# Optimization experiments

Hardware: AMD Instinct MI355X
Metric: run time of the kernel (lower is better)

The kernel has to match this reference:

```python
import jax, jax.numpy as jnp
import numpy as np
from jax import lax

B, T, IDIM, HDIM = 128, 256, 64, 128
TS, KS, OC1, ANF = 64, 3, 100, 64
S1 = TS - 3 * (KS - 1)   # 58: three VALID ks=3 stride-1 convs
S = S1 * S1              # 3364
HN = 2 * HDIM            # 256 = h_dim * l_dim (l_dim=2)
F = S + HN               # 3620
HID = F // 2             # 1810


def _conv(x, w, b):
    y = lax.conv_general_dilated(x, w, (1, 1), 'VALID',
                                 dimension_numbers=('NCHW', 'OIHW', 'NCHW'))
    return y + b[None, :, None, None]


def _lstm_layer(x, w_ih, w_hh, b_ih, b_hh):
    # x: [B, T, D] -> (outputs [B, T, H], final hidden [B, H]); PyTorch gate order i,f,g,o
    Bn = x.shape[0]
    h0 = jnp.zeros((Bn, HDIM), x.dtype)
    c0 = jnp.zeros((Bn, HDIM), x.dtype)
    def step(carry, xt):
        h, c = carry
        g = xt @ w_ih.T + h @ w_hh.T + b_ih + b_hh
        i, f, gg, o = jnp.split(g, 4, axis=-1)
        c = jax.nn.sigmoid(f) * c + jax.nn.sigmoid(i) * jnp.tanh(gg)
        h = jax.nn.sigmoid(o) * jnp.tanh(c)
        return (h, c), h
    (hT, cT), ys = lax.scan(step, (h0, c0), jnp.swapaxes(x, 0, 1))
    return jnp.swapaxes(ys, 0, 1), hT


def setup_inputs() -> dict:
    key = jax.random.key(0)
    k = jax.random.split(key, 30)
    s = 0.05
    H4 = 4 * HDIM
    return {
        'x1': jax.random.normal(k[0], (B, 3, TS, TS), jnp.float32),
        'x2': jax.random.normal(k[1], (B, T, IDIM), jnp.float32),
        # conv2a/conv2b: two Monte-Carlo weight samples of the same Bayesian conv2 layer
        'conv1_w': jax.random.normal(k[2], (OC1, 3, KS, KS), jnp.float32) * s,
        'conv1_b': jax.random.normal(k[3], (OC1,), jnp.float32) * s,
        'conv2a_w': jax.random.normal(k[4], (OC1, OC1, KS, KS), jnp.float32) * s,
        'conv2a_b': jax.random.normal(k[5], (OC1,), jnp.float32) * s,
        'conv2b_w': jax.random.normal(k[6], (OC1, OC1, KS, KS), jnp.float32) * s,
        'conv2b_b': jax.random.normal(k[7], (OC1,), jnp.float32) * s,
        'w_ih0': jax.random.normal(k[8], (H4, IDIM), jnp.float32) * s,
        'w_hh0': jax.random.normal(k[9], (H4, HDIM), jnp.float32) * s,
        'b_ih0': jax.random.normal(k[10], (H4,), jnp.float32) * s,
        'b_hh0': jax.random.normal(k[11], (H4,), jnp.float32) * s,
        'w_ih1': jax.random.normal(k[12], (H4, HDIM), jnp.float32) * s,
        'w_hh1': jax.random.normal(k[13], (H4, HDIM), jnp.float32) * s,
        'b_ih1': jax.random.normal(k[14], (H4,), jnp.float32) * s,
        'b_hh1': jax.random.normal(k[15], (H4,), jnp.float32) * s,
        'attn1_w': jax.random.normal(k[16], (ANF, F), jnp.float32) * s,
        'attn1_b': jax.random.normal(k[17], (ANF,), jnp.float32) * s,
        'attn2_w': jax.random.normal(k[18], (1, ANF), jnp.float32) * s,
        'attn2_b': jax.random.normal(k[19], (1,), jnp.float32) * s,
        'fc1_w': jax.random.normal(k[20], (HID, F), jnp.float32) * s,
        'fc1_b': jax.random.normal(k[21], (HID,), jnp.float32) * s,
        'fc2_w': jax.random.normal(k[22], (1, HID), jnp.float32) * s,
        'fc2_b': jax.random.normal(k[23], (1,), jnp.float32) * s,
    }


def reference(x1, x2, conv1_w, conv1_b, conv2a_w, conv2a_b, conv2b_w, conv2b_b,
              w_ih0, w_hh0, b_ih0, b_hh0, w_ih1, w_hh1, b_ih1, b_hh1,
              attn1_w, attn1_b, attn2_w, attn2_b, fc1_w, fc1_b, fc2_w, fc2_b):
    Bn = x1.shape[0]
    # CNN branch
    x = jax.nn.relu(_conv(x1, conv1_w, conv1_b))
    x = jax.nn.relu(_conv(x, conv2a_w, conv2a_b))
    x = jax.nn.relu(_conv(x, conv2b_w, conv2b_b))
    xd = x.reshape(Bn, OC1, S)                               # [B, oc1, S]
    # LSTM branch (2 layers, dropout in eval mode = identity)
    y0, h0f = _lstm_layer(x2, w_ih0, w_hh0, b_ih0, b_hh0)
    _, h1f = _lstm_layer(y0, w_ih1, w_hh1, b_ih1, b_hh1)
    hn = jnp.concatenate([h0f, h1f], axis=1)                 # [B, 2*h_dim]
    # Broadcast hidden state across channels (replaces the torch concat loop)
    hn_b = jnp.broadcast_to(hn[:, None, :], (Bn, OC1, HN))
    fused = jnp.concatenate([xd, hn_b], axis=2)              # [B, oc1, F]
    # Attention
    a = jnp.tanh(fused @ attn1_w.T + attn1_b)                # [B, oc1, anf]
    a = a @ attn2_w.T + attn2_b                              # [B, oc1, 1]
    a = jax.nn.softmax(a, axis=1)
    ctx = jnp.einsum('bcs,bco->bso', xd, a).reshape(Bn, S)   # [B, S]
    # Fusion MLP (dropout eval-mode identity)
    m = jnp.concatenate([ctx, hn], axis=1)                   # [B, F]
    h = jax.nn.relu(m @ fc1_w.T + fc1_b)
    return h @ fc2_w.T + fc2_b                               # [B, 1]
```

## Files before the change

### kernel.cpp

```cpp
#include <hip/hip_runtime.h>
#include <hip/hip_bf16.h>
#include <math.h>

#define BB 128
#define TT 256
#define IDIM 64
#define HD 128
#define G4 512
#define OC 100
#define W1 62
#define W2 60
#define W3 58
#define NPX1 (W1*W1)
#define NPX2 (W2*W2)
#define NPX3 (W3*W3)
#define SS NPX3
#define FF (SS + 2*HD)
#define HIDN 1810
#define ANF 64

typedef __hip_bfloat16 bf16;
typedef _Float16 f16;
typedef __attribute__((ext_vector_type(8))) short bf16x8;
typedef __attribute__((ext_vector_type(4))) short bf16x4;
typedef __attribute__((ext_vector_type(2))) _Float16 half2v;
typedef __attribute__((ext_vector_type(4))) float f32x4;

__device__ __forceinline__ float ldf(const float* p) { return *p; }
__device__ __forceinline__ float ldf(const bf16* p)  { return __bfloat162float(*p); }
__device__ __forceinline__ void  stf(float* p, float v) { *p = v; }
__device__ __forceinline__ void  stf(bf16* p, float v)  { *p = __float2bfloat16(v); }

__device__ __forceinline__ short f2bs(float v) {
    bf16 t = __float2bfloat16(v); short s; __builtin_memcpy(&s, &t, 2); return s;
}
__device__ __forceinline__ float fsig(float x) {
    return __builtin_amdgcn_rcpf(1.f + __expf(-x));
}
__device__ __forceinline__ float ftanh(float x) {
    float t = __expf(-2.f * fabsf(x));
    float r = __builtin_amdgcn_rcpf(1.f + t);
    float m = 1.f - 2.f * t * r;
    return copysignf(m, x);
}
__device__ __forceinline__ float fmix2(unsigned w, unsigned h, float acc) {
    half2v wv, hv;
    __builtin_memcpy(&wv, &w, 4);
    __builtin_memcpy(&hv, &h, 4);
    acc = fmaf((float)wv[0], (float)hv[0], acc);
    acc = fmaf((float)wv[1], (float)hv[1], acc);
    return acc;
}

__device__ __forceinline__ bf16x8 load8(const bf16* p) { return *(const bf16x8*)p; }
__device__ __forceinline__ bf16x8 load8(const float* p) {
    float4 x = *(const float4*)p;
    float4 y = *(const float4*)(p + 4);
    bf16x8 r;
    r[0] = f2bs(x.x); r[1] = f2bs(x.y); r[2] = f2bs(x.z); r[3] = f2bs(x.w);
    r[4] = f2bs(y.x); r[5] = f2bs(y.y); r[6] = f2bs(y.z); r[7] = f2bs(y.w);
    return r;
}

__global__ void zero_kernel(float* o, int n)
{
    int i = blockIdx.x * 256 + threadIdx.x;
    if (i < n) o[i] = 0.f;
}

__global__ __launch_bounds__(256)
void cvt4_bf16(const float* __restrict__ s, bf16* __restrict__ d, int n4)
{
    int i = blockIdx.x * 256 + threadIdx.x;
    if (i >= n4) return;
    float4 v = ((const float4*)s)[i];
    bf16x4 o;
    o[0] = f2bs(v.x); o[1] = f2bs(v.y); o[2] = f2bs(v.z); o[3] = f2bs(v.w);
    *(bf16x4*)(d + 4 * (size_t)i) = o;
}

__global__ __launch_bounds__(256)
void cvt4_f16(const float* __restrict__ s, f16* __restrict__ d, int n4)
{
    int i = blockIdx.x * 256 + threadIdx.x;
    if (i >= n4) return;
    float4 v = ((const float4*)s)[i];
    f16 o[4] = {(f16)v.x, (f16)v.y, (f16)v.z, (f16)v.w};
    *(uint2*)(d + 4 * (size_t)i) = *(uint2*)o;
}

__global__ __launch_bounds__(256)
void conv1_kernel(const float* __restrict__ x1,
                  const float* __restrict__ w,
                  const float* __restrict__ bias,
                  bf16* __restrict__ out)
{
    __shared__ float wl[2700];
    __shared__ float bl[OC];
    int tid = threadIdx.x;
    for (int i = tid; i < 2700; i += 256) wl[i] = w[i];
    if (tid < OC) bl[tid] = bias[tid];
    __syncthreads();
    int b  = blockIdx.x;
    int px = blockIdx.y * 256 + tid;
    if (px >= NPX1) return;
    int y = px / W1, x = px % W1;
    float in[3][3][3];
    const float* xb = x1 + (size_t)b * 3 * 64 * 64;
#pragma unroll
    for (int ic = 0; ic < 3; ic++)
#pragma unroll
        for (int r = 0; r < 3; r++)
#pragma unroll
            for (int c = 0; c < 3; c++)
                in[ic][r][c] = xb[(ic * 64 + y + r) * 64 + x + c];
    bf16* ob = out + (size_t)b * OC * NPX1 + px;
    for (int oc = 0; oc < OC; ++oc) {
        float acc = bl[oc];
        const float* wp = &wl[oc * 27];
#pragma unroll
        for (int ic = 0; ic < 3; ic++)
#pragma unroll
            for (int r = 0; r < 3; r++)
#pragma unroll
                for (int c = 0; c < 3; c++)
                    acc = fmaf(in[ic][r][c], wp[ic * 9 + r * 3 + c], acc);
        ob[(size_t)oc * NPX1] = __float2bfloat16(fmaxf(acc, 0.f));
    }
}

__global__ __launch_bounds__(256)
void wt_repack(const float* __restrict__ w, bf16* __restrict__ WT)
{
    int idx = blockIdx.x * 256 + threadIdx.x;
    if (idx >= 129024) return;
    int i  = idx & 31;
    int oc = (idx >> 5) % 112;
    int ts = idx / (112 * 32);
    int s = ts & 3, t = ts >> 2;
    int ic = s * 32 + i;
    float v = 0.f;
    if (oc < OC && ic < OC) v = w[(oc * OC + ic) * 9 + t];
    WT[idx] = __float2bfloat16(v);
}

__global__ __launch_bounds__(512, 1)
void conv2_mfma(const bf16* __restrict__ in,
                const bf16* __restrict__ WT,
                const float* __restrict__ bias,
                bf16* __restrict__ out,
                int iw, int ow)
{
    __shared__ bf16 il[10 * 72 * 40];
    __shared__ bf16 wl[4032 * 8];
    int tid = threadIdx.x;
    int b = blockIdx.x;
    int y0 = blockIdx.y * 8;
    int wid = tid >> 6;
    int l = tid & 63;
    int hq = l >> 4;
    int l16 = l & 15;
    int yo = y0 + wid;

    f32x4 acc[7][4];
#pragma unroll
    for (int f = 0; f < 7; f++) {
#pragma unroll
        for (int r = 0; r < 4; r++) {
            int oc = f * 16 + hq * 4 + r;
            float bv = (oc < OC) ? bias[oc] : 0.f;
#pragma unroll
            for (int n = 0; n < 4; n++) acc[f][n][r] = bv;
        }
    }

    const size_t ims = (size_t)iw * iw;
    int icl = tid & 31;
    int t2  = tid >> 5;
    for (int s = 0; s < 4; ++s) {
        __syncthreads();
        int ic = s * 32 + icl;
        bool icok = ic < OC;
        const bf16* ibase = in + (size_t)(b * OC + ic) * ims;
#pragma unroll
        for (int it = 0; it < 6; ++it) {
            int u2 = t2 + it * 16;
            if (u2 < 90) {
                int r = u2 / 9, xb = u2 - r * 9;
                int x8 = xb * 8;
                int yy = y0 + r;
                bf16x8 v = {0, 0, 0, 0, 0, 0, 0, 0};
                if (icok && yy < iw && x8 < iw) {
                    const short* sp = (const short*)(ibase + (size_t)yy * iw + x8);
                    if (x8 + 8 <= iw) {
                        const unsigned* sp32 = (const unsigned*)sp;
#pragma unroll
                        for (int q = 0; q < 4; q++)
                            ((unsigned*)&v)[q] = sp32[q];
                    } else {
                        for (int k = 0; k < 8; k++)
                            if (x8 + k < iw) ((short*)&v)[k] = sp[k];
                    }
                }
                bf16* dst = &il[(r * 72 + x8) * 40 + icl];
#pragma unroll
                for (int k = 0; k < 8; k++)
                    *(short*)&dst[k * 40] = ((short*)&v)[k];
            }
        }
#pragma unroll
        for (int it = 0; it < 8; ++it) {
            int u = tid + it * 512;
            if (u < 4032) {
                int t = u / 448; int rem = u - t * 448;
                int oc = rem >> 2; int hq2 = rem & 3;
                *(bf16x8*)&wl[(size_t)((t * 4 + hq2) * 112 + oc) * 8] =
                    *(const bf16x8*)(WT + (size_t)((t * 4 + s) * 112 + oc) * 32 + hq2 * 8);
            }
        }
        __syncthreads();

#pragma unroll
        for (int ky = 0; ky < 3; ++ky) {
#pragma unroll
            for (int kx = 0; kx < 3; ++kx) {
                int t = ky * 3 + kx;
                bf16x8 a[7];
#pragma unroll
                for (int f = 0; f < 7; f++)
                    a[f] = *(const bf16x8*)&wl[(size_t)((t * 4 + hq) * 112 + f * 16 + l16) * 8];
                bf16x8 bfr[4];
#pragma unroll
                for (int n = 0; n < 4; n++)
                    bfr[n] = *(const bf16x8*)&il[((wid + ky) * 72 + kx + l16 + n * 16) * 40 + hq * 8];
#pragma unroll
                for (int f = 0; f < 7; f++)
#pragma unroll
                    for (int n = 0; n < 4; n++)
                        acc[f][n] = __builtin_amdgcn_mfma_f32_16x16x32_bf16(
                            a[f], bfr[n], acc[f][n], 0, 0, 0);
            }
        }
    }

    if (yo < ow) {
#pragma unroll
        for (int f = 0; f < 7; f++) {
#pragma unroll
            for (int r = 0; r < 4; r++) {
                int oc = f * 16 + hq * 4 + r;
                if (oc < OC) {
#pragma unroll
                    for (int n = 0; n < 4; n++) {
                        int x = n * 16 + l16;
                        if (x < ow)
                            out[((size_t)(b * OC + oc) * ow + yo) * ow + x] =
                                __float2bfloat16(fmaxf(acc[f][n][r], 0.f));
                    }
                }
            }
        }
    }
}

template<typename TB, typename TC, int ACT>
__global__ __launch_bounds__(256)
void gemm_mfma(const bf16* __restrict__ A, int lda,
               const TB* __restrict__ B, int ldb,
               const float* __restrict__ bias,
               TC* __restrict__ C, int ldc,
               int M, int N, int K)
{
    __shared__ bf16 As[64 * 72];
    __shared__ bf16 Bs[64 * 72];
    int tid = threadIdx.x;
    int l = tid & 63, wid = tid >> 6;
    int l16 = l & 15, h = l >> 4;
    int m0 = blockIdx.x * 64, n0 = blockIdx.y * 64;
    f32x4 acc[4];
#pragma unroll
    for (int nb = 0; nb < 4; nb++) acc[nb] = (f32x4){0.f, 0.f, 0.f, 0.f};

    int rs = tid >> 3;
    int kc = (tid & 7) * 8;

    for (int k0 = 0; k0 < K; k0 += 64) {
        int kr = K - k0;
#pragma unroll
        for (int half = 0; half < 2; half++) {
            int rr = rs + half * 32;
            bf16x8 av = {0, 0, 0, 0, 0, 0, 0, 0};
            int m = m0 + rr;
            if (m < M) {
                const short* src = (const short*)(A + (size_t)m * lda + k0 + kc);
                if (kc + 8 <= kr) av = *(const bf16x8*)src;
                else if (kc < kr) {
                    for (int j = 0; j < 8; j++) if (kc + j < kr) ((short*)&av)[j] = src[j];
                }
            }
            *(bf16x8*)&As[rr * 72 + kc] = av;
            bf16x8 bv = {0, 0, 0, 0, 0, 0, 0, 0};
            int n = n0 + rr;
            if (n < N) {
                const TB* src = B + (size_t)n * ldb + k0 + kc;
                if (kc + 8 <= kr) bv = load8(src);
                else if (kc < kr) {
                    for (int j = 0; j < 8; j++) if (kc + j < kr) ((short*)&bv)[j] = f2bs(ldf(src + j));
                }
            }
            *(bf16x8*)&Bs[rr * 72 + kc] = bv;
        }
        __syncthreads();
#pragma unroll
        for (int kk = 0; kk < 2; kk++) {
            bf16x8 af = *(const bf16x8*)&As[(wid * 16 + l16) * 72 + kk * 32 + h * 8];
#pragma unroll
            for (int nb = 0; nb < 4; nb++) {
                bf16x8 bfr = *(const bf16x8*)&Bs[(nb * 16 + l16) * 72 + kk * 32 + h * 8];
                acc[nb] = __builtin_amdgcn_mfma_f32_16x16x32_bf16(af, bfr, acc[nb], 0, 0, 0);
            }
        }
        __syncthreads();
    }
#pragma unroll
    for (int nb = 0; nb < 4; nb++) {
        int col = n0 + nb * 16 + l16;
        if (col >= N) continue;
        float bv = bias ? bias[col] : 0.f;
#pragma unroll
        for (int reg = 0; reg < 4; reg++) {
            int row = m0 + wid * 16 + h * 4 + reg;
            if (row < M) {
                float v = acc[nb][reg] + bv;
                if (ACT == 1) v = fmaxf(v, 0.f);
                stf(&C[(size_t)row * ldc + col], v);
            }
        }
    }
}

template<typename TA, typename TC, int BM, int BN, int BK, int TM, int TN, int ACT>
__global__ __launch_bounds__((BM / TM) * (BN / TN))
void gemm_tn(const TA* __restrict__ A, int lda,
             const float* __restrict__ Bmat, int ldb,
             const float* __restrict__ bias,
             TC* __restrict__ C, int ldc,
             int M, int N, int K)
{
    constexpr int TX = BN / TN;
    constexpr int TY = BM / TM;
    constexpr int NT = TX * TY;
    __shared__ float As[BK][BM + 1];
    __shared__ float Bs[BK][BN + 1];
    int tid = threadIdx.x;
    int tx = tid % TX, ty = tid / TX;
    int m0 = blockIdx.x * BM, n0 = blockIdx.y * BN;
    float acc[TM][TN] = {};
    for (int k0 = 0; k0 < K; k0 += BK) {
        for (int idx = tid; idx < BM * BK; idx += NT) {
            int i = idx / BK, j = idx % BK;
            int m = m0 + i, k = k0 + j;
            As[j][i] = (m < M && k < K) ? ldf(&A[(size_t)m * lda + k]) : 0.f;
        }
        for (int idx = tid; idx < BN * BK; idx += NT) {
            int i = idx / BK, j = idx % BK;
            int n = n0 + i, k = k0 + j;
            Bs[j][i] = (n < N && k < K) ? Bmat[(size_t)n * ldb + k] : 0.f;
        }
        __syncthreads();
#pragma unroll
        for (int k = 0; k < BK; ++k) {
            float av[TM], bv[TN];
#pragma unroll
            for (int i = 0; i < TM; i++) av[i] = As[k][ty * TM + i];
#pragma unroll
            for (int j = 0; j < TN; j++) bv[j] = Bs[k][tx * TN + j];
#pragma unroll
            for (int i = 0; i < TM; i++)
#pragma unroll
                for (int j = 0; j < TN; j++)
                    acc[i][j] += av[i] * bv[j];
        }
        __syncthreads();
    }
#pragma unroll
    for (int i = 0; i < TM; i++) {
        int m = m0 + ty * TM + i;
        if (m >= M) continue;
#pragma unroll
        for (int j = 0; j < TN; j++) {
            int n = n0 + tx * TN + j;
            if (n >= N) continue;
            float v = acc[i][j] + (bias ? bias[n] : 0.f);
            if (ACT == 1) v = fmaxf(v, 0.f);
            stf(&C[(size_t)m * ldc + n], v);
        }
    }
}

__global__ __launch_bounds__(512, 1)
void lstm_recur(const bf16* __restrict__ G,
                const f16* __restrict__ LWr,
                bf16* __restrict__ Y,
                float* __restrict__ HN,
                int hoff)
{
    __shared__ __align__(16) f16 hl[HD];
    __shared__ float ex[G4];
    int g = threadIdx.x;
    int b = blockIdx.x;
    uint4 wv[16];
    const uint4* wp = (const uint4*)(LWr + (size_t)g * HD);
#pragma unroll
    for (int q = 0; q < 16; q++) wv[q] = wp[q];
#pragma unroll
    for (int q = 0; q < 16; q++)
        asm volatile("" : "+v"(wv[q].x), "+v"(wv[q].y), "+v"(wv[q].z), "+v"(wv[q].w));
    float c = 0.f;
    if (g < HD) hl[g] = (f16)0.f;
    __syncthreads();
    const bf16* Gb = G + (size_t)b * TT * G4 + g;
    for (int t = 0; t < TT; ++t) {
        float dot = __bfloat162float(Gb[(size_t)t * G4]);
        float a0 = 0.f, a1 = 0.f, a2 = 0.f, a3 = 0.f;
#pragma unroll
        for (int q = 0; q < 16; q++) {
            uint4 hw = *(const uint4*)&hl[q * 8];
            a0 = fmix2(wv[q].x, hw.x, a0);
            a1 = fmix2(wv[q].y, hw.y, a1);
            a2 = fmix2(wv[q].z, hw.z, a2);
            a3 = fmix2(wv[q].w, hw.w, a3);
        }
        dot += (a0 + a1) + (a2 + a3);
        float tr;
        if (g < 2 * HD || g >= 3 * HD) tr = fsig(dot);
        else tr = ftanh(dot);
        ex[g] = tr;
        __syncthreads();
        if (g < HD) {
            float iv = ex[g], fv = ex[HD + g], gv = ex[2 * HD + g], ov = ex[3 * HD + g];
            c = fv * c + iv * gv;
            float nh = ov * ftanh(c);
            hl[g] = (f16)nh;
            if (Y) Y[((size_t)b * TT + t) * HD + g] = __float2bfloat16(nh);
            if (t == TT - 1) HN[(size_t)b * 256 + hoff + g] = nh;
        }
        __syncthreads();
    }
}

__global__ void bias_sum(const float* a, const float* b, float* o, int n)
{
    int i = blockIdx.x * 256 + threadIdx.x;
    if (i < n) o[i] = a[i] + b[i];
}

__global__ __launch_bounds__(128)
void attn_softmax(const float* __restrict__ T1,
                  const float* __restrict__ HB,
                  const float* __restrict__ a2w,
                  const float* __restrict__ a2b,
                  float* __restrict__ ATT)
{
    __shared__ float hbl[ANF];
    __shared__ float awl[ANF];
    __shared__ float red[128];
    int b = blockIdx.x, tid = threadIdx.x;
    if (tid < ANF) { hbl[tid] = HB[b * ANF + tid]; awl[tid] = a2w[tid]; }
    __syncthreads();
    float lg = -1e30f;
    if (tid < OC) {
        const float* tp = T1 + (size_t)(b * OC + tid) * ANF;
        float s = 0.f;
#pragma unroll 4
        for (int j = 0; j < ANF; j++) s += ftanh(tp[j] + hbl[j]) * awl[j];
        lg = s + a2b[0];
    }
    red[tid] = lg; __syncthreads();
    for (int st = 64; st > 0; st >>= 1) { if (tid < st) red[tid] = fmaxf(red[tid], red[tid + st]); __syncthreads(); }
    float mx = red[0]; __syncthreads();
    float e = (tid < OC) ? __expf(lg - mx) : 0.f;
    red[tid] = e; __syncthreads();
    for (int st = 64; st > 0; st >>= 1) { if (tid < st) red[tid] += red[tid + st]; __syncthreads(); }
    if (tid < OC) ATT[b * OC + tid] = e / red[0];
}

__global__ __launch_bounds__(256)
void ctx_concat(const bf16* __restrict__ XD,
                const float* __restrict__ ATT,
                const float* __restrict__ HN,
                bf16* __restrict__ M)
{
    __shared__ float al[OC];
    int b = blockIdx.x;
    int tid = threadIdx.x;
    if (tid < OC) al[tid] = ATT[b * OC + tid];
    __syncthreads();
    int s = blockIdx.y * 256 + tid;
    if (s < SS) {
        const bf16* xp = XD + (size_t)b * OC * SS + s;
        float acc = 0.f;
#pragma unroll 4
        for (int c = 0; c < OC; c++) acc = fmaf(__bfloat162float(xp[(size_t)c * SS]), al[c], acc);
        M[(size_t)b * FF + s] = __float2bfloat16(acc);
    } else if (s < FF) {
        M[(size_t)b * FF + s] = __float2bfloat16(HN[b * 256 + (s - SS)]);
    }
}

__global__ __launch_bounds__(256)
void fc2_kernel(const float* __restrict__ H1,
                const float* __restrict__ w,
                const float* __restrict__ bias,
                float* __restrict__ out)
{
    int tid = threadIdx.x;
    int lane = tid & 63, wid = tid >> 6;
    int b = blockIdx.x * 4 + wid;
    float acc = 0.f;
    for (int j = lane; j < HIDN; j += 64) acc = fmaf(H1[(size_t)b * HIDN + j], w[j], acc);
#pragma unroll
    for (int off = 32; off > 0; off >>= 1) acc += __shfl_down(acc, off, 64);
    if (lane == 0) out[b] = acc + bias[0];
}

extern "C" void kernel_launch(void* const* d_in, const int* in_sizes, int n_in,
                              void* d_out, int out_size, void* d_ws, size_t ws_size,
                              hipStream_t stream)
{
    const float* x1   = (const float*)d_in[0];
    const float* x2   = (const float*)d_in[1];
    const float* c1w  = (const float*)d_in[2];
    const float* c1b  = (const float*)d_in[3];
    const float* c2aw = (const float*)d_in[4];
    const float* c2ab = (const float*)d_in[5];
    const float* c2bw = (const float*)d_in[6];
    const float* c2bb = (const float*)d_in[7];
    const float* wih0 = (const float*)d_in[8];
    const float* whh0 = (const float*)d_in[9];
    const float* bih0 = (const float*)d_in[10];
    const float* bhh0 = (const float*)d_in[11];
    const float* wih1 = (const float*)d_in[12];
    const float* whh1 = (const float*)d_in[13];
    const float* bih1 = (const float*)d_in[14];
    const float* bhh1 = (const float*)d_in[15];
    const float* a1w  = (const float*)d_in[16];
    const float* a1b  = (const float*)d_in[17];
    const float* a2w  = (const float*)d_in[18];
    const float* a2b  = (const float*)d_in[19];
    const float* f1w  = (const float*)d_in[20];
    const float* f1b  = (const float*)d_in[21];
    const float* f2w  = (const float*)d_in[22];
    const float* f2b  = (const float*)d_in[23];
    float* out = (float*)d_out;

    char* base = (char*)d_ws;
    bf16* G0    = (bf16*)(base + 0);
    bf16* Y0    = (bf16*)(base + 33554432);
    bf16* G1    = G0;
    bf16* X2B   = (bf16*)(base + 41943040);
    bf16* WIH0B = (bf16*)(base + 46137344);
    bf16* WIH1B = (bf16*)(base + 46202880);
    f16*  LWf0  = (f16*)(base + 46333952);
    f16*  LWf1  = (f16*)(base + 46465024);
    const size_t LSTM_END = 46596096;

    int nb = 0; size_t ov = 0;
    for (int cand = BB; cand >= 32; cand >>= 1) {
        size_t cnn = (size_t)cand * OC * (NPX1 + NPX2) * 2;
        size_t o = cnn > LSTM_END ? cnn : LSTM_END;
        size_t q = o + 2048 + 2048 + 131072 + 32768
                 + (size_t)cand * OC * 64 * 4
                 + (((size_t)cand * OC * 4 + 255) & ~(size_t)255)
                 + 926720 + 926720 + 258048 + 258048 + 463360;
        if (ws_size >= q) { nb = cand; ov = o; break; }
    }
    if (nb == 0) {
        zero_kernel<<<1, 128, 0, stream>>>(out, out_size);
        return;
    }
    bf16* A1c = (bf16*)(base + 0);
    bf16* A2c = (bf16*)(base + (size_t)nb * OC * NPX1 * 2);
    bf16* XDc = A1c;
    size_t p = ov;
    float* BS0  = (float*)(base + p); p += 2048;
    float* BS1  = (float*)(base + p); p += 2048;
    float* HN   = (float*)(base + p); p += 131072;
    float* HB   = (float*)(base + p); p += 32768;
    float* T1c  = (float*)(base + p); p += (size_t)nb * OC * 64 * 4;
    float* ATTc = (float*)(base + p); p += ((size_t)nb * OC * 4 + 255) & ~(size_t)255;
    bf16*  MBb  = (bf16*)(base + p); p += 926720;
    float* H1   = (float*)(base + p); p += 926720;
    bf16* WTa   = (bf16*)(base + p); p += 258048;
    bf16* WTb   = (bf16*)(base + p); p += 258048;
    bf16* A1WB  = (bf16*)(base + p); p += 463360;

    wt_repack<<<504, 256, 0, stream>>>(c2aw, WTa);
    wt_repack<<<504, 256, 0, stream>>>(c2bw, WTb);
    cvt4_f16<<<64,   256, 0, stream>>>(whh0, LWf0, 16384);
    cvt4_f16<<<64,   256, 0, stream>>>(whh1, LWf1, 16384);
    cvt4_bf16<<<2048, 256, 0, stream>>>(x2,   X2B,   524288);
    cvt4_bf16<<<32,   256, 0, stream>>>(wih0, WIH0B, 8192);
    cvt4_bf16<<<64,   256, 0, stream>>>(wih1, WIH1B, 16384);
    cvt4_bf16<<<227,  256, 0, stream>>>(a1w,  A1WB,  57920);
    bias_sum<<<2, 256, 0, stream>>>(bih0, bhh0, BS0, G4);
    bias_sum<<<2, 256, 0, stream>>>(bih1, bhh1, BS1, G4);

    gemm_mfma<bf16, bf16, 0><<<dim3(512, 8), 256, 0, stream>>>(
        X2B, IDIM, WIH0B, IDIM, BS0, G0, G4, BB * TT, G4, IDIM);
    lstm_recur<<<BB, 512, 0, stream>>>(G0, LWf0, Y0, HN, 0);
    gemm_mfma<bf16, bf16, 0><<<dim3(512, 8), 256, 0, stream>>>(
        Y0, HD, WIH1B, HD, BS1, G1, G4, BB * TT, G4, HD);
    lstm_recur<<<BB, 512, 0, stream>>>(G1, LWf1, (bf16*)nullptr, HN, HD);

    gemm_tn<float, float, 32, 32, 16, 2, 2, 0><<<dim3(4, 2), 256, 0, stream>>>(
        HN, 256, a1w + SS, FF, a1b, HB, ANF, BB, ANF, 256);

    for (int c0 = 0; c0 < BB; c0 += nb) {
        conv1_kernel<<<dim3(nb, 16), 256, 0, stream>>>(
            x1 + (size_t)c0 * 3 * 64 * 64, c1w, c1b, A1c);
        conv2_mfma<<<dim3(nb, 8), 512, 0, stream>>>(A1c, WTa, c2ab, A2c, W1, W2);
        conv2_mfma<<<dim3(nb, 8), 512, 0, stream>>>(A2c, WTb, c2bb, XDc, W2, W3);
        gemm_mfma<bf16, float, 0><<<dim3(nb * OC / 64, 1), 256, 0, stream>>>(
            XDc, SS, A1WB, FF, nullptr, T1c, ANF, nb * OC, ANF, SS);
        attn_softmax<<<nb, 128, 0, stream>>>(T1c, HB + (size_t)c0 * ANF, a2w, a2b, ATTc);
        ctx_concat<<<dim3(nb, 15), 256, 0, stream>>>(
            XDc, ATTc, HN + (size_t)c0 * 256, MBb + (size_t)c0 * FF);
    }

    gemm_mfma<float, float, 1><<<dim3(2, 29), 256, 0, stream>>>(
        MBb, FF, f1w, FF, f1b, H1, HIDN, BB, HIDN, FF);
    fc2_kernel<<<BB / 4, 256, 0, stream>>>(H1, f2w, f2b, out);
}
```

Measured before the change: 1.229 ms.

## Double-buffer LSTM state to drop a barrier; relayout conv weight LDS tiles

The LSTM recurrence now keeps double-buffered hidden-state and gate arrays in shared memory, so each timestep needs only one __syncthreads instead of two. Every wave redundantly computes the cell update for two hidden units per lane, and only wave 0 writes the outputs. Separately, the conv kernel stores its weight tile in LDS in MFMA fragment order, so each lane reads contiguous 16-byte chunks, which is meant to cut bank conflicts. The cost is redundant cell-state arithmetic in all eight waves and extra shared memory.

Result: no change. 1.241 ms (+0.9%).

```diff
diff --git a/kernel.cpp b/kernel.cpp
--- a/kernel.cpp
+++ b/kernel.cpp
@@ -212,9 +212,11 @@
         for (int it = 0; it < 8; ++it) {
             int u = tid + it * 512;
             if (u < 4032) {
-                int t = u / 448; int rem = u - t * 448;
-                int oc = rem >> 2; int hq2 = rem & 3;
-                *(bf16x8*)&wl[(size_t)((t * 4 + hq2) * 112 + oc) * 8] =
+                int tf = u >> 6; int lp = u & 63;
+                int t = tf / 7, f = tf - t * 7;
+                int oc = f * 16 + (lp & 15);
+                int hq2 = lp >> 4;
+                *(bf16x8*)&wl[(size_t)u * 8] =
                     *(const bf16x8*)(WT + (size_t)((t * 4 + s) * 112 + oc) * 32 + hq2 * 8);
             }
         }
@@ -228,7 +230,7 @@
                 bf16x8 a[7];
 #pragma unroll
                 for (int f = 0; f < 7; f++)
-                    a[f] = *(const bf16x8*)&wl[(size_t)((t * 4 + hq) * 112 + f * 16 + l16) * 8];
+                    a[f] = *(const bf16x8*)&wl[(size_t)((t * 7 + f) * 64 + l) * 8];
                 bf16x8 bfr[4];
 #pragma unroll
                 for (int n = 0; n < 4; n++)
@@ -405,10 +407,12 @@
                 float* __restrict__ HN,
                 int hoff)
 {
-    __shared__ __align__(16) f16 hl[HD];
-    __shared__ float ex[G4];
+    __shared__ __align__(16) f16 hbuf[2][HD];
+    __shared__ __align__(16) float ex[2][G4];
     int g = threadIdx.x;
     int b = blockIdx.x;
+    int lane = g & 63;
+    int w = g >> 6;
     uint4 wv[16];
     const uint4* wp = (const uint4*)(LWr + (size_t)g * HD);
 #pragma unroll
@@ -416,16 +420,19 @@
 #pragma unroll
     for (int q = 0; q < 16; q++)
         asm volatile("" : "+v"(wv[q].x), "+v"(wv[q].y), "+v"(wv[q].z), "+v"(wv[q].w));
-    float c = 0.f;
-    if (g < HD) hl[g] = (f16)0.f;
+    float c0 = 0.f, c1 = 0.f;
+    if (g < HD) hbuf[0][g] = (f16)0.f;
     __syncthreads();
     const bf16* Gb = G + (size_t)b * TT * G4 + g;
+    bool hasY = (Y != nullptr);
     for (int t = 0; t < TT; ++t) {
+        int rb = t & 1;
         float dot = __bfloat162float(Gb[(size_t)t * G4]);
         float a0 = 0.f, a1 = 0.f, a2 = 0.f, a3 = 0.f;
+        const f16* hr = hbuf[rb];
 #pragma unroll
         for (int q = 0; q < 16; q++) {
-            uint4 hw = *(const uint4*)&hl[q * 8];
+            uint4 hw = *(const uint4*)&hr[q * 8];
             a0 = fmix2(wv[q].x, hw.x, a0);
             a1 = fmix2(wv[q].y, hw.y, a1);
             a2 = fmix2(wv[q].z, hw.z, a2);
@@ -435,17 +442,28 @@
         float tr;
         if (g < 2 * HD || g >= 3 * HD) tr = fsig(dot);
         else tr = ftanh(dot);
-        ex[g] = tr;
+        ex[rb][g] = tr;
         __syncthreads();
-        if (g < HD) {
-            float iv = ex[g], fv = ex[HD + g], gv = ex[2 * HD + g], ov = ex[3 * HD + g];
-            c = fv * c + iv * gv;
-            float nh = ov * ftanh(c);
-            hl[g] = (f16)nh;
-            if (Y) Y[((size_t)b * TT + t) * HD + g] = __float2bfloat16(nh);
-            if (t == TT - 1) HN[(size_t)b * 256 + hoff + g] = nh;
-        }
-        __syncthreads();
+        float2 iv = *(const float2*)&ex[rb][2 * lane];
+        float2 fv = *(const float2*)&ex[rb][HD + 2 * lane];
+        float2 gv = *(const float2*)&ex[rb][2 * HD + 2 * lane];
+        float2 ov = *(const float2*)&ex[rb][3 * HD + 2 * lane];
+        c0 = fv.x * c0 + iv.x * gv.x;
+        c1 = fv.y * c1 + iv.y * gv.y;
+        float h0 = ov.x * ftanh(c0);
+        float h1 = ov.y * ftanh(c1);
+        f16 hp[2] = {(f16)h0, (f16)h1};
+        *(unsigned*)&hbuf[rb ^ 1][2 * lane] = *(unsigned*)hp;
+        if (w == 0) {
+            if (hasY) {
+                short yb[2] = {f2bs(h0), f2bs(h1)};
+                *(unsigned*)(Y + ((size_t)b * TT + t) * HD + 2 * lane) = *(unsigned*)yb;
+            }
+            if (t == TT - 1) {
+                float2 hn; hn.x = h0; hn.y = h1;
+                *(float2*)&HN[(size_t)b * 256 + hoff + 2 * lane] = hn;
+            }
+        }
     }
 }
 
```
